# Performance work log

Hardware: AMD Instinct MI355X
Metric: run time of the kernel (lower is better)

## Reference

```python
import jax, jax.numpy as jnp
import numpy as np

B, S, D, H = 4, 4096, 2048, 16
DH = D // H
SCALE = float(np.sqrt(DH))


def setup_inputs() -> dict:
    key = jax.random.key(0)
    ks = jax.random.split(key, 11)
    std = 1.0 / np.sqrt(D)
    inp = {
        "query": jax.random.normal(ks[0], (B, S, D), jnp.float32),
        "key": jax.random.normal(ks[1], (B, S, D), jnp.float32),
        "value": jax.random.normal(ks[2], (B, S, D), jnp.float32),
        "Wq": jax.random.normal(ks[3], (D, D), jnp.float32) * std,
        "bq": jax.random.normal(ks[4], (D,), jnp.float32) * std,
        "Wk": jax.random.normal(ks[5], (D, D), jnp.float32) * std,
        "bk": jax.random.normal(ks[6], (D,), jnp.float32) * std,
        "Wv": jax.random.normal(ks[7], (D, D), jnp.float32) * std,
        "bv": jax.random.normal(ks[8], (D,), jnp.float32) * std,
        "Wo": jax.random.normal(ks[9], (D, D), jnp.float32) * std,
        "bo": jax.random.normal(ks[10], (D,), jnp.float32) * std,
    }
    return inp


def reference(query, key, value, Wq, bq, Wk, bk, Wv, bv, Wo, bo):
    # Linear projections (torch nn.Linear: x @ W^T + b)
    Q = query @ Wq.T + bq          # [B,S,D]
    K = key @ Wk.T + bk
    V = value @ Wv.T + bv
    Q = Q.reshape(B, S, H, DH)
    K = K.reshape(B, S, H, DH)
    V = V.reshape(B, S, H, DH)
    # NOTE: original torch code does NOT transpose heads to dim 1, so the
    # matmul contracts over head-dim pairs at each position: scores [B,S,H,H]
    scores = jnp.einsum('bsid,bsjd->bsij', Q, K) / SCALE
    attention = jax.nn.softmax(scores, axis=-1)   # softmax over heads (faithful)
    x = jnp.einsum('bsij,bsjd->bsid', attention, V)  # [B,S,H,DH]
    # permute(0,2,1,3) -> [B,H,S,DH], then view(B,-1,D) -> [B,S,D]
    x = jnp.transpose(x, (0, 2, 1, 3)).reshape(B, S, D)
    out = x @ Wo.T + bo
    return out, attention
```

## Files before the change

kernel.cpp:

```cpp
#include <hip/hip_runtime.h>


#define DEV __device__ __forceinline__

using short8  = __attribute__((ext_vector_type(8))) short;
using ushort8 = __attribute__((ext_vector_type(8))) unsigned short;
using f32x4   = __attribute__((ext_vector_type(4))) float;
using u16x8   = __attribute__((ext_vector_type(8))) unsigned short;

constexpr int BATCH = 4, SEQ = 4096, DIM = 2048;
constexpr int GM = BATCH * SEQ;
constexpr int GN = DIM, GK = DIM;

DEV unsigned short f2bf(float f) {
  unsigned int u = __builtin_bit_cast(unsigned int, f);
  u += 0x7FFFu + ((u >> 16) & 1u);
  return (unsigned short)(u >> 16);
}
DEV float bf2f(unsigned short h) {
  unsigned int u = ((unsigned int)h) << 16;
  return __builtin_bit_cast(float, u);
}

DEV void gload16(const void* g, void* l) {
  __builtin_amdgcn_global_load_lds(
      (const __attribute__((address_space(1))) void*)g,
      (__attribute__((address_space(3))) void*)l, 16, 0, 0);
}

#define BAR    __builtin_amdgcn_s_barrier()
#define LGKM0  asm volatile("s_waitcnt lgkmcnt(0)" ::: "memory")
#define LGKM(N) asm volatile("s_waitcnt lgkmcnt(" #N ")" ::: "memory")
#define VMC(N) asm volatile("s_waitcnt vmcnt(" #N ")" ::: "memory")
#define SCHED0 __builtin_amdgcn_sched_barrier(0)
#define PRIO1  __builtin_amdgcn_s_setprio(1)
#define PRIO0  __builtin_amdgcn_s_setprio(0)
#define MFMA16(a, b, c) __builtin_amdgcn_mfma_f32_16x16x32_bf16(a, b, c, 0, 0, 0)

#define QUAD(AF, BF, MO, NO)                                          \
  _Pragma("unroll") for (int m_ = 0; m_ < 4; ++m_)                    \
  _Pragma("unroll") for (int n_ = 0; n_ < 4; ++n_) {                  \
    acc[(MO) + m_][(NO) + n_] =                                       \
        MFMA16(AF[m_][0], BF[n_][0], acc[(MO) + m_][(NO) + n_]);      \
    acc[(MO) + m_][(NO) + n_] =                                       \
        MFMA16(AF[m_][1], BF[n_][1], acc[(MO) + m_][(NO) + n_]);      \
  }

constexpr size_t NE_C = (size_t)GM * GK;
constexpr size_t WE_C = (size_t)GK * GN;

__global__ __launch_bounds__(256)
void cvt_all(const float* __restrict__ q, const float* __restrict__ k,
             const float* __restrict__ v, const float* __restrict__ Wq,
             const float* __restrict__ Wk, const float* __restrict__ Wv,
             const float* __restrict__ Wo,
             unsigned short* __restrict__ Qin, unsigned short* __restrict__ Kin,
             unsigned short* __restrict__ Vin, unsigned short* __restrict__ Wqb,
             unsigned short* __restrict__ Wkb, unsigned short* __restrict__ Wvb,
             unsigned short* __restrict__ Wob) {
  size_t gi = ((size_t)blockIdx.x * 256 + threadIdx.x) * 8;
  const float* src;
  unsigned short* dst;
  size_t off;
  if (gi < NE_C)            { src = q;  dst = Qin; off = gi; }
  else if (gi < 2 * NE_C)   { src = k;  dst = Kin; off = gi - NE_C; }
  else if (gi < 3 * NE_C)   { src = v;  dst = Vin; off = gi - 2 * NE_C; }
  else {
    size_t w = gi - 3 * NE_C;
    if (w < WE_C)           { src = Wq; dst = Wqb; off = w; }
    else if (w < 2 * WE_C)  { src = Wk; dst = Wkb; off = w - WE_C; }
    else if (w < 3 * WE_C)  { src = Wv; dst = Wvb; off = w - 2 * WE_C; }
    else                    { src = Wo; dst = Wob; off = w - 3 * WE_C; }
  }
  f32x4 f0 = *(const f32x4*)(src + off);
  f32x4 f1 = *(const f32x4*)(src + off + 4);
  ushort8 o;
#pragma unroll
  for (int j = 0; j < 4; ++j) { o[j] = f2bf(f0[j]); o[4 + j] = f2bf(f1[j]); }
  *(ushort8*)(dst + off) = o;
}

template <bool OUTF32>
__global__ __launch_bounds__(256, 1)
void gemm256p(const unsigned short* __restrict__ Ap,
              const unsigned short* __restrict__ Bp,
              const float* __restrict__ bias, void* __restrict__ Cp) {
  constexpr int BK = 64, KT = GK / BK;
  __shared__ unsigned short As[2][256 * BK];
  __shared__ unsigned short Bs[2][256 * BK];

  const int tid  = threadIdx.x;
  const int lane = tid & 63;
  const int wv   = tid >> 6;
  const int wm   = wv >> 1, wn = wv & 1;

  int bid = (int)blockIdx.x;
  const int xcd = bid & 7, rr = bid >> 3;
  const int gg = rr >> 5, jj = rr & 31;
  const int mt = xcd * 8 + gg * 4 + (jj & 3);
  const int nt = jj >> 2;
  const int bm0 = mt * 256, bn0 = nt * 256;

  int offA[8];
#pragma unroll
  for (int r = 0; r < 8; ++r) {
    int d = tid * 16 + r * 4096;
    int s = d ^ (((d >> 7) & 7) << 4);
    int row = s >> 7, col = (s & 127) >> 1;
    offA[r] = (bm0 + row) * GK + col;
  }
  const int dAB = (bn0 - bm0) * GK;

  const int r16 = lane & 15, kb = (lane >> 4) * 16;

  f32x4 acc[8][8] = {};
  short8 al[4][2], ah[4][2], bl[4][2], bh[4][2];

  auto stA = [&](int buf, int T) {
#pragma unroll
    for (int r = 0; r < 8; ++r)
      gload16(Ap + (size_t)offA[r] + (size_t)T * BK,
              (char*)&As[buf][0] + (tid * 16 + r * 4096));
  };
  auto stB = [&](int buf, int T) {
#pragma unroll
    for (int r = 0; r < 8; ++r)
      gload16(Bp + (size_t)(offA[r] + dAB) + (size_t)T * BK,
              (char*)&Bs[buf][0] + (tid * 16 + r * 4096));
  };
  auto ldf = [&](const unsigned short* base, int row, int ks) -> short8 {
    int a = (row * 128 + ks * 64 + kb) ^ ((row & 7) << 4);
    return *(const short8*)((const char*)base + a);
  };
  auto rdS = [&](short8 (&dst)[4][2], const unsigned short* base, int row0) {
#pragma unroll
    for (int m = 0; m < 4; ++m) {
      dst[m][0] = ldf(base, row0 + m * 16 + r16, 0);
      dst[m][1] = ldf(base, row0 + m * 16 + r16, 1);
    }
  };

  stA(0, 0); stB(0, 0);
  VMC(0); SCHED0; BAR;
  stA(1, 1); stB(1, 1);
  rdS(al, &As[0][0], wm * 128);
  rdS(bl, &Bs[0][0], wn * 128);

  for (int T = 0; T < KT; ++T) {
    const int bb = T & 1;
    const unsigned short* Ac = &As[bb][0];
    const unsigned short* Bc = &Bs[bb][0];
    const unsigned short* An = &As[bb ^ 1][0];
    const unsigned short* Bn = &Bs[bb ^ 1][0];
    const bool m1 = (T + 1 < KT), m2 = (T + 2 < KT);

    rdS(bh, Bc, wn * 128 + 64);
    LGKM(8); SCHED0;
    PRIO1; QUAD(al, bl, 0, 0); PRIO0;

    rdS(ah, Ac, wm * 128 + 64);
    LGKM(8); SCHED0;
    PRIO1; QUAD(al, bh, 0, 4); PRIO0;

    LGKM0; SCHED0;
    if (m1) {
      if (m2) { VMC(8); } else { VMC(0); }
      SCHED0; BAR;
      if (m2) stA(bb, T + 2);
      rdS(al, An, wm * 128);
    }
    PRIO1; QUAD(ah, bh, 4, 4); PRIO0;

    if (m1) {
      if (m2) { VMC(8); } else { VMC(0); }
      SCHED0; BAR;
      if (m2) stB(bb, T + 2);
    }
    PRIO1; QUAD(ah, bl, 4, 0); PRIO0;
    if (m1) rdS(bl, Bn, wn * 128);
  }

  float bs[8];
#pragma unroll
  for (int n = 0; n < 8; ++n) bs[n] = bias[bn0 + wn * 128 + n * 16 + r16];
  const int rb = (lane >> 4) * 4;
#pragma unroll
  for (int m = 0; m < 8; ++m)
#pragma unroll
    for (int i = 0; i < 4; ++i) {
      const size_t row = (size_t)bm0 + wm * 128 + m * 16 + rb + i;
#pragma unroll
      for (int n = 0; n < 8; ++n) {
        const int col = bn0 + wn * 128 + n * 16 + r16;
        float v = acc[m][n][i] + bs[n];
        if constexpr (OUTF32)
          ((float*)Cp)[row * GN + col] = v;
        else
          ((unsigned short*)Cp)[row * GN + col] = f2bf(v);
      }
    }
}

__global__ __launch_bounds__(256)
void attn_kernel(const unsigned short* __restrict__ Qb,
                 const unsigned short* __restrict__ Kb,
                 const unsigned short* __restrict__ Vb,
                 float* __restrict__ attnOut,
                 unsigned short* __restrict__ X2) {
  __shared__ float qf[16 * 128];
  __shared__ float kf[16 * 132];
  __shared__ float vf[16 * 128];
  __shared__ float sc[256];

  const int t = threadIdx.x;
  const int p = blockIdx.x;
  const size_t rowoff = (size_t)p * DIM;

  {
    const int e = t * 8;
    u16x8 qv = *(const u16x8*)(Qb + rowoff + e);
    u16x8 kv = *(const u16x8*)(Kb + rowoff + e);
    u16x8 vv = *(const u16x8*)(Vb + rowoff + e);
    const int r = t >> 4, c = (t & 15) * 8;
#pragma unroll
    for (int j = 0; j < 8; ++j) qf[r * 128 + c + j] = bf2f(qv[j]);
#pragma unroll
    for (int j = 0; j < 8; ++j) kf[r * 132 + c + j] = bf2f(kv[j]);
#pragma unroll
    for (int j = 0; j < 8; ++j) vf[r * 128 + c + j] = bf2f(vv[j]);
  }
  __syncthreads();

  const int i = t >> 4, j = t & 15;
  float s = 0.f;
#pragma unroll
  for (int d4 = 0; d4 < 32; ++d4) {
    f32x4 q4 = *(const f32x4*)&qf[i * 128 + d4 * 4];
    f32x4 k4 = *(const f32x4*)&kf[j * 132 + d4 * 4];
    s = fmaf(q4[0], k4[0], fmaf(q4[1], k4[1], fmaf(q4[2], k4[2], fmaf(q4[3], k4[3], s))));
  }
  s *= 0.08838834764831845f;

  float mx = s;
#pragma unroll
  for (int off = 8; off; off >>= 1) mx = fmaxf(mx, __shfl_xor(mx, off, 16));
  float ex = __expf(s - mx);
  float sum = ex;
#pragma unroll
  for (int off = 8; off; off >>= 1) sum += __shfl_xor(sum, off, 16);
  float a = ex / sum;

  attnOut[(size_t)p * 256 + t] = a;
  sc[t] = a;
  __syncthreads();

  const int dh0 = j * 8;
  float o[8] = {};
#pragma unroll
  for (int jjq = 0; jjq < 16; ++jjq) {
    float aij = sc[i * 16 + jjq];
#pragma unroll
    for (int e2 = 0; e2 < 8; ++e2)
      o[e2] = fmaf(aij, vf[jjq * 128 + dh0 + e2], o[e2]);
  }
  const int b = p >> 12, spos = p & 4095;
  const int row = i * 256 + (spos >> 4);
  const int col = ((spos & 15) << 7) + dh0;
  ushort8 pk;
#pragma unroll
  for (int e2 = 0; e2 < 8; ++e2) pk[e2] = f2bf(o[e2]);
  *(ushort8*)(X2 + (size_t)b * (SEQ * DIM) + (size_t)row * DIM + col) = pk;
}

extern "C" void kernel_launch(void* const* d_in, const int* in_sizes, int n_in,
                              void* d_out, int out_size, void* d_ws,
                              size_t ws_size, hipStream_t stream) {
  const float* q  = (const float*)d_in[0];
  const float* k  = (const float*)d_in[1];
  const float* v  = (const float*)d_in[2];
  const float* Wq = (const float*)d_in[3];
  const float* bq = (const float*)d_in[4];
  const float* Wk = (const float*)d_in[5];
  const float* bk = (const float*)d_in[6];
  const float* Wv = (const float*)d_in[7];
  const float* bv = (const float*)d_in[8];
  const float* Wo = (const float*)d_in[9];
  const float* bo = (const float*)d_in[10];

  const size_t NE = NE_C;
  const size_t WE = WE_C;

  unsigned short* ws16 = (unsigned short*)d_ws;
  unsigned short* Wq_b = ws16;
  unsigned short* Wk_b = Wq_b + WE;
  unsigned short* Wv_b = Wk_b + WE;
  unsigned short* Wo_b = Wv_b + WE;
  unsigned short* Qb   = Wo_b + WE;
  unsigned short* Kb   = Qb + NE;
  unsigned short* Vb   = Kb + NE;
  unsigned short* X2   = Vb + NE;
  unsigned short* Qin  = X2 + NE;
  unsigned short* Kin  = Qin + NE;
  unsigned short* Vin  = Kin + NE;

  float* outMain = (float*)d_out;
  float* attnOut = outMain + (size_t)GM * GN;

  const int cvt_blocks = (int)((3 * NE + 4 * WE) / 8 / 256);
  cvt_all<<<cvt_blocks, 256, 0, stream>>>(q, k, v, Wq, Wk, Wv, Wo,
                                          Qin, Kin, Vin, Wq_b, Wk_b, Wv_b, Wo_b);

  constexpr int G256 = (GM / 256) * (GN / 256);

  gemm256p<false><<<G256, 256, 0, stream>>>(Qin, Wq_b, bq, Qb);
  gemm256p<false><<<G256, 256, 0, stream>>>(Kin, Wk_b, bk, Kb);
  gemm256p<false><<<G256, 256, 0, stream>>>(Vin, Wv_b, bv, Vb);

  attn_kernel<<<GM, 256, 0, stream>>>(Qb, Kb, Vb, attnOut, X2);

  gemm256p<true><<<G256, 256, 0, stream>>>(X2, Wo_b, bo, outMain);
}
```

Before: 950.7 us.

## Pre-swizzle weights into MFMA fragment layout and load B directly to registers

The weight conversion kernel now writes the weights in an MFMA-fragment-ordered layout, so each wave can load its B operand straight from global memory into registers. The LDS staging path for B is dropped. The GEMM tile shrinks from 256x256 to 128x128, uses a triple-buffered LDS ring for A only, and targets two blocks per CU. This cuts LDS traffic and barriers and raises occupancy, at the cost of more global B reads per tile and a smaller per-block reuse footprint.

```diff
diff --git a/kernel.cpp b/kernel.cpp
--- a/kernel.cpp
+++ b/kernel.cpp
@@ -29,174 +29,177 @@
 }
 
 #define BAR    __builtin_amdgcn_s_barrier()
-#define LGKM0  asm volatile("s_waitcnt lgkmcnt(0)" ::: "memory")
-#define LGKM(N) asm volatile("s_waitcnt lgkmcnt(" #N ")" ::: "memory")
 #define VMC(N) asm volatile("s_waitcnt vmcnt(" #N ")" ::: "memory")
 #define SCHED0 __builtin_amdgcn_sched_barrier(0)
 #define PRIO1  __builtin_amdgcn_s_setprio(1)
 #define PRIO0  __builtin_amdgcn_s_setprio(0)
 #define MFMA16(a, b, c) __builtin_amdgcn_mfma_f32_16x16x32_bf16(a, b, c, 0, 0, 0)
 
-#define QUAD(AF, BF, MO, NO)                                          \
-  _Pragma("unroll") for (int m_ = 0; m_ < 4; ++m_)                    \
-  _Pragma("unroll") for (int n_ = 0; n_ < 4; ++n_) {                  \
-    acc[(MO) + m_][(NO) + n_] =                                       \
-        MFMA16(AF[m_][0], BF[n_][0], acc[(MO) + m_][(NO) + n_]);      \
-    acc[(MO) + m_][(NO) + n_] =                                       \
-        MFMA16(AF[m_][1], BF[n_][1], acc[(MO) + m_][(NO) + n_]);      \
-  }
-
 constexpr size_t NE_C = (size_t)GM * GK;
 constexpr size_t WE_C = (size_t)GK * GN;
 
 __global__ __launch_bounds__(256)
-void cvt_all(const float* __restrict__ q, const float* __restrict__ k,
-             const float* __restrict__ v, const float* __restrict__ Wq,
-             const float* __restrict__ Wk, const float* __restrict__ Wv,
-             const float* __restrict__ Wo,
-             unsigned short* __restrict__ Qin, unsigned short* __restrict__ Kin,
-             unsigned short* __restrict__ Vin, unsigned short* __restrict__ Wqb,
-             unsigned short* __restrict__ Wkb, unsigned short* __restrict__ Wvb,
-             unsigned short* __restrict__ Wob) {
-  size_t gi = ((size_t)blockIdx.x * 256 + threadIdx.x) * 8;
-  const float* src;
-  unsigned short* dst;
-  size_t off;
-  if (gi < NE_C)            { src = q;  dst = Qin; off = gi; }
-  else if (gi < 2 * NE_C)   { src = k;  dst = Kin; off = gi - NE_C; }
-  else if (gi < 3 * NE_C)   { src = v;  dst = Vin; off = gi - 2 * NE_C; }
-  else {
-    size_t w = gi - 3 * NE_C;
-    if (w < WE_C)           { src = Wq; dst = Wqb; off = w; }
-    else if (w < 2 * WE_C)  { src = Wk; dst = Wkb; off = w - WE_C; }
-    else if (w < 3 * WE_C)  { src = Wv; dst = Wvb; off = w - 2 * WE_C; }
-    else                    { src = Wo; dst = Wob; off = w - 3 * WE_C; }
-  }
-  f32x4 f0 = *(const f32x4*)(src + off);
-  f32x4 f1 = *(const f32x4*)(src + off + 4);
-  ushort8 o;
-#pragma unroll
-  for (int j = 0; j < 4; ++j) { o[j] = f2bf(f0[j]); o[4 + j] = f2bf(f1[j]); }
-  *(ushort8*)(dst + off) = o;
+void prep(const float* __restrict__ q, const float* __restrict__ k,
+          const float* __restrict__ v, const float* __restrict__ Wq,
+          const float* __restrict__ Wk, const float* __restrict__ Wv,
+          const float* __restrict__ Wo,
+          unsigned short* __restrict__ Qin, unsigned short* __restrict__ Kin,
+          unsigned short* __restrict__ Vin, unsigned short* __restrict__ Bq,
+          unsigned short* __restrict__ Bk, unsigned short* __restrict__ Bv,
+          unsigned short* __restrict__ Bo) {
+  const int bid = blockIdx.x;
+  if (bid < 49152) {
+    const int tens = bid >> 14;
+    const size_t off = ((size_t)(bid & 16383) * 256 + threadIdx.x) * 8;
+    const float* s = tens == 0 ? q : tens == 1 ? k : v;
+    unsigned short* d = tens == 0 ? Qin : tens == 1 ? Kin : Vin;
+    f32x4 f0 = *(const f32x4*)(s + off);
+    f32x4 f1 = *(const f32x4*)(s + off + 4);
+    ushort8 o;
+#pragma unroll
+    for (int j = 0; j < 4; ++j) { o[j] = f2bf(f0[j]); o[4 + j] = f2bf(f1[j]); }
+    *(ushort8*)(d + off) = o;
+  } else {
+    const int wb = bid - 49152;
+    const int w = wb >> 11;
+    const int t = (wb & 2047) * 256 + threadIdx.x;
+    const float* W = w == 0 ? Wq : w == 1 ? Wk : w == 2 ? Wv : Wo;
+    unsigned short* D = w == 0 ? Bq : w == 1 ? Bk : w == 2 ? Bv : Bo;
+    const int lane = t & 63, f = (t >> 6) & 7, half = (t >> 9) & 1;
+    const int kt = (t >> 10) & 31, nt = t >> 15;
+    const int n  = nt * 128 + half * 64 + (f >> 1) * 16 + (lane & 15);
+    const int kk = kt * 64 + (f & 1) * 32 + (lane >> 4) * 8;
+    const float* sp = W + (size_t)n * GK + kk;
+    f32x4 f0 = *(const f32x4*)sp;
+    f32x4 f1 = *(const f32x4*)(sp + 4);
+    ushort8 o;
+#pragma unroll
+    for (int j = 0; j < 4; ++j) { o[j] = f2bf(f0[j]); o[4 + j] = f2bf(f1[j]); }
+    *(ushort8*)(D + (size_t)t * 8) = o;
+  }
 }
 
 template <bool OUTF32>
-__global__ __launch_bounds__(256, 1)
-void gemm256p(const unsigned short* __restrict__ Ap,
-              const unsigned short* __restrict__ Bp,
+__global__ __launch_bounds__(256, 2)
+void gemm128d(const unsigned short* __restrict__ Ap,
+              const unsigned short* __restrict__ Bf,
               const float* __restrict__ bias, void* __restrict__ Cp) {
   constexpr int BK = 64, KT = GK / BK;
-  __shared__ unsigned short As[2][256 * BK];
-  __shared__ unsigned short Bs[2][256 * BK];
+  __shared__ unsigned short As[3][128 * 64];
 
   const int tid  = threadIdx.x;
   const int lane = tid & 63;
   const int wv   = tid >> 6;
   const int wm   = wv >> 1, wn = wv & 1;
 
-  int bid = (int)blockIdx.x;
+  const int bid = (int)blockIdx.x;
   const int xcd = bid & 7, rr = bid >> 3;
-  const int gg = rr >> 5, jj = rr & 31;
-  const int mt = xcd * 8 + gg * 4 + (jj & 3);
-  const int nt = jj >> 2;
-  const int bm0 = mt * 256, bn0 = nt * 256;
-
-  int offA[8];
-#pragma unroll
-  for (int r = 0; r < 8; ++r) {
+  const int gg = rr >> 6, jj = rr & 63;
+  const int mt = xcd * 16 + (gg >> 1) * 8 + (jj & 7);
+  const int nt = (gg & 1) * 8 + (jj >> 3);
+  const int bm0 = mt * 128, bn0 = nt * 128;
+
+  int offA[4];
+#pragma unroll
+  for (int r = 0; r < 4; ++r) {
     int d = tid * 16 + r * 4096;
     int s = d ^ (((d >> 7) & 7) << 4);
-    int row = s >> 7, col = (s & 127) >> 1;
-    offA[r] = (bm0 + row) * GK + col;
-  }
-  const int dAB = (bn0 - bm0) * GK;
-
+    offA[r] = (bm0 + (s >> 7)) * GK + ((s & 127) >> 1);
+  }
   const int r16 = lane & 15, kb = (lane >> 4) * 16;
 
-  f32x4 acc[8][8] = {};
-  short8 al[4][2], ah[4][2], bl[4][2], bh[4][2];
-
-  auto stA = [&](int buf, int T) {
-#pragma unroll
-    for (int r = 0; r < 8; ++r)
+  const unsigned short* Bw =
+      Bf + (size_t)nt * KT * 8192 + (size_t)wn * 4096 + (size_t)lane * 8;
+
+  f32x4 acc[4][4] = {};
+  short8 afA[4][2], afB[4][2], bA[4][2], bB[4][2];
+
+  auto stA = [&](int bufoff, int T) {
+#pragma unroll
+    for (int r = 0; r < 4; ++r)
       gload16(Ap + (size_t)offA[r] + (size_t)T * BK,
-              (char*)&As[buf][0] + (tid * 16 + r * 4096));
-  };
-  auto stB = [&](int buf, int T) {
-#pragma unroll
-    for (int r = 0; r < 8; ++r)
-      gload16(Bp + (size_t)(offA[r] + dAB) + (size_t)T * BK,
-              (char*)&Bs[buf][0] + (tid * 16 + r * 4096));
-  };
-  auto ldf = [&](const unsigned short* base, int row, int ks) -> short8 {
-    int a = (row * 128 + ks * 64 + kb) ^ ((row & 7) << 4);
-    return *(const short8*)((const char*)base + a);
-  };
-  auto rdS = [&](short8 (&dst)[4][2], const unsigned short* base, int row0) {
-#pragma unroll
-    for (int m = 0; m < 4; ++m) {
-      dst[m][0] = ldf(base, row0 + m * 16 + r16, 0);
-      dst[m][1] = ldf(base, row0 + m * 16 + r16, 1);
+              (char*)&As[0][0] + bufoff + (tid * 16 + r * 4096));
+  };
+  auto loadB = [&](short8 (&b)[4][2], int T) {
+    const unsigned short* p = Bw + (size_t)T * 8192;
+#pragma unroll
+    for (int f = 0; f < 8; ++f) {
+      asm volatile("global_load_dwordx4 %0, %1, off"
+                   : "=v"(b[f >> 1][f & 1]) : "v"(p + f * 512) : "memory");
     }
   };
-
-  stA(0, 0); stB(0, 0);
-  VMC(0); SCHED0; BAR;
-  stA(1, 1); stB(1, 1);
-  rdS(al, &As[0][0], wm * 128);
-  rdS(bl, &Bs[0][0], wn * 128);
-
-  for (int T = 0; T < KT; ++T) {
-    const int bb = T & 1;
-    const unsigned short* Ac = &As[bb][0];
-    const unsigned short* Bc = &Bs[bb][0];
-    const unsigned short* An = &As[bb ^ 1][0];
-    const unsigned short* Bn = &Bs[bb ^ 1][0];
-    const bool m1 = (T + 1 < KT), m2 = (T + 2 < KT);
-
-    rdS(bh, Bc, wn * 128 + 64);
-    LGKM(8); SCHED0;
-    PRIO1; QUAD(al, bl, 0, 0); PRIO0;
-
-    rdS(ah, Ac, wm * 128 + 64);
-    LGKM(8); SCHED0;
-    PRIO1; QUAD(al, bh, 0, 4); PRIO0;
-
-    LGKM0; SCHED0;
-    if (m1) {
-      if (m2) { VMC(8); } else { VMC(0); }
-      SCHED0; BAR;
-      if (m2) stA(bb, T + 2);
-      rdS(al, An, wm * 128);
+  auto rdA = [&](short8 (&a)[4][2], int bufoff) {
+#pragma unroll
+    for (int m = 0; m < 4; ++m)
+#pragma unroll
+      for (int ks = 0; ks < 2; ++ks) {
+        int row = wm * 64 + m * 16 + r16;
+        int ad = (row * 128 + ks * 64 + kb) ^ ((row & 7) << 4);
+        a[m][ks] = *(const short8*)((const char*)&As[0][0] + bufoff + ad);
+      }
+  };
+  auto cluster = [&](short8 (&a)[4][2], short8 (&b)[4][2]) {
+    PRIO1;
+#pragma unroll
+    for (int m = 0; m < 4; ++m)
+#pragma unroll
+      for (int n = 0; n < 4; ++n) {
+        acc[m][n] = MFMA16(a[m][0], b[n][0], acc[m][n]);
+        acc[m][n] = MFMA16(a[m][1], b[n][1], acc[m][n]);
+      }
+    PRIO0;
+  };
+
+  auto body = [&](int T, short8 (&cb)[4][2], short8 (&nb)[4][2],
+                  short8 (&ca)[4][2], short8 (&na)[4][2],
+                  int bufn, int bufs) {
+    if (T + 1 < KT) loadB(nb, T + 1);
+    SCHED0;
+    if (T + 2 < KT) stA(bufs, T + 2);
+    SCHED0;
+    if (T + 2 < KT)      { VMC(12); }
+    else if (T + 1 < KT) { VMC(8); }
+    else                 { VMC(0); }
+    SCHED0;
+    if (T + 1 < KT) {
+      BAR; SCHED0;
+      rdA(na, bufn);
+      SCHED0;
     }
-    PRIO1; QUAD(ah, bh, 4, 4); PRIO0;
-
-    if (m1) {
-      if (m2) { VMC(8); } else { VMC(0); }
-      SCHED0; BAR;
-      if (m2) stB(bb, T + 2);
-    }
-    PRIO1; QUAD(ah, bl, 4, 0); PRIO0;
-    if (m1) rdS(bl, Bn, wn * 128);
-  }
-
-  float bs[8];
-#pragma unroll
-  for (int n = 0; n < 8; ++n) bs[n] = bias[bn0 + wn * 128 + n * 16 + r16];
+    cluster(ca, cb);
+  };
+
+  stA(0, 0); stA(16384, 1);
+  loadB(bA, 0);
+  SCHED0; VMC(12); SCHED0;
+  BAR; SCHED0;
+  rdA(afA, 0);
+  SCHED0;
+
+  int b0 = 0, b1 = 16384, b2 = 32768;
+  for (int T = 0; T < KT; T += 2) {
+    body(T,     bA, bB, afA, afB, b1, b2);
+    body(T + 1, bB, bA, afB, afA, b2, b0);
+    int tmp = b2; b2 = b1; b1 = b0; b0 = tmp;
+  }
+
+  float bs[4];
+#pragma unroll
+  for (int n = 0; n < 4; ++n) bs[n] = bias[bn0 + wn * 64 + n * 16 + r16];
   const int rb = (lane >> 4) * 4;
 #pragma unroll
-  for (int m = 0; m < 8; ++m)
+  for (int m = 0; m < 4; ++m)
 #pragma unroll
     for (int i = 0; i < 4; ++i) {
-      const size_t row = (size_t)bm0 + wm * 128 + m * 16 + rb + i;
-#pragma unroll
-      for (int n = 0; n < 8; ++n) {
-        const int col = bn0 + wn * 128 + n * 16 + r16;
-        float v = acc[m][n][i] + bs[n];
+      const size_t row = (size_t)bm0 + wm * 64 + m * 16 + rb + i;
+#pragma unroll
+      for (int n = 0; n < 4; ++n) {
+        const int col = bn0 + wn * 64 + n * 16 + r16;
+        float val = acc[m][n][i] + bs[n];
         if constexpr (OUTF32)
-          ((float*)Cp)[row * GN + col] = v;
+          ((float*)Cp)[row * GN + col] = val;
         else
-          ((unsigned short*)Cp)[row * GN + col] = f2bf(v);
+          ((unsigned short*)Cp)[row * GN + col] = f2bf(val);
       }
     }
 }
@@ -287,15 +290,14 @@
   const float* Wo = (const float*)d_in[9];
   const float* bo = (const float*)d_in[10];
 
-  const size_t NE = NE_C;
-  const size_t WE = WE_C;
+  const size_t NE = NE_C, WE = WE_C;
 
   unsigned short* ws16 = (unsigned short*)d_ws;
-  unsigned short* Wq_b = ws16;
-  unsigned short* Wk_b = Wq_b + WE;
-  unsigned short* Wv_b = Wk_b + WE;
-  unsigned short* Wo_b = Wv_b + WE;
-  unsigned short* Qb   = Wo_b + WE;
+  unsigned short* Bq_f = ws16;
+  unsigned short* Bk_f = Bq_f + WE;
+  unsigned short* Bv_f = Bk_f + WE;
+  unsigned short* Bo_f = Bv_f + WE;
+  unsigned short* Qb   = Bo_f + WE;
   unsigned short* Kb   = Qb + NE;
   unsigned short* Vb   = Kb + NE;
   unsigned short* X2   = Vb + NE;
@@ -306,17 +308,16 @@
   float* outMain = (float*)d_out;
   float* attnOut = outMain + (size_t)GM * GN;
 
-  const int cvt_blocks = (int)((3 * NE + 4 * WE) / 8 / 256);
-  cvt_all<<<cvt_blocks, 256, 0, stream>>>(q, k, v, Wq, Wk, Wv, Wo,
-                                          Qin, Kin, Vin, Wq_b, Wk_b, Wv_b, Wo_b);
-
-  constexpr int G256 = (GM / 256) * (GN / 256);
-
-  gemm256p<false><<<G256, 256, 0, stream>>>(Qin, Wq_b, bq, Qb);
-  gemm256p<false><<<G256, 256, 0, stream>>>(Kin, Wk_b, bk, Kb);
-  gemm256p<false><<<G256, 256, 0, stream>>>(Vin, Wv_b, bv, Vb);
+  prep<<<57344, 256, 0, stream>>>(q, k, v, Wq, Wk, Wv, Wo,
+                                  Qin, Kin, Vin, Bq_f, Bk_f, Bv_f, Bo_f);
+
+  constexpr int G128 = (GM / 128) * (GN / 128);
+
+  gemm128d<false><<<G128, 256, 0, stream>>>(Qin, Bq_f, bq, Qb);
+  gemm128d<false><<<G128, 256, 0, stream>>>(Kin, Bk_f, bk, Kb);
+  gemm128d<false><<<G128, 256, 0, stream>>>(Vin, Bv_f, bv, Vb);
 
   attn_kernel<<<GM, 256, 0, stream>>>(Qb, Kb, Vb, attnOut, X2);
 
-  gemm256p<true><<<G256, 256, 0, stream>>>(X2, Wo_b, bo, outMain);
-}
+  gemm128d<true><<<G128, 256, 0, stream>>>(X2, Bo_f, bo, outMain);
+}
```

Result: faster. 817.0 us (-14.1%).

## Rework projection GEMM into 8-wave four-stage pipeline and fuse QKV launches

Applied to the files above, without the earlier changes.

Replaces the 4-wave, double-buffered 256x256 GEMM (BK=64) with an 8-wave version that uses BK=32 and a four-buffer pipeline. Loads are prefetched three k-steps ahead and each wave computes a 128x64 sub-tile. The three Q/K/V projections now run as one launch that picks its tensor from the block index, which removes launch gaps and tail effects between them. The trade-off is more barriers per k-step and 128KB of LDS, so the requested two blocks per CU likely cannot both fit.

```diff
diff --git a/kernel.cpp b/kernel.cpp
--- a/kernel.cpp
+++ b/kernel.cpp
@@ -30,21 +30,11 @@
 
 #define BAR    __builtin_amdgcn_s_barrier()
 #define LGKM0  asm volatile("s_waitcnt lgkmcnt(0)" ::: "memory")
-#define LGKM(N) asm volatile("s_waitcnt lgkmcnt(" #N ")" ::: "memory")
 #define VMC(N) asm volatile("s_waitcnt vmcnt(" #N ")" ::: "memory")
 #define SCHED0 __builtin_amdgcn_sched_barrier(0)
 #define PRIO1  __builtin_amdgcn_s_setprio(1)
 #define PRIO0  __builtin_amdgcn_s_setprio(0)
 #define MFMA16(a, b, c) __builtin_amdgcn_mfma_f32_16x16x32_bf16(a, b, c, 0, 0, 0)
-
-#define QUAD(AF, BF, MO, NO)                                          \
-  _Pragma("unroll") for (int m_ = 0; m_ < 4; ++m_)                    \
-  _Pragma("unroll") for (int n_ = 0; n_ < 4; ++n_) {                  \
-    acc[(MO) + m_][(NO) + n_] =                                       \
-        MFMA16(AF[m_][0], BF[n_][0], acc[(MO) + m_][(NO) + n_]);      \
-    acc[(MO) + m_][(NO) + n_] =                                       \
-        MFMA16(AF[m_][1], BF[n_][1], acc[(MO) + m_][(NO) + n_]);      \
-  }
 
 constexpr size_t NE_C = (size_t)GM * GK;
 constexpr size_t WE_C = (size_t)GK * GN;
@@ -80,109 +70,119 @@
   *(ushort8*)(dst + off) = o;
 }
 
-template <bool OUTF32>
-__global__ __launch_bounds__(256, 1)
-void gemm256p(const unsigned short* __restrict__ Ap,
-              const unsigned short* __restrict__ Bp,
-              const float* __restrict__ bias, void* __restrict__ Cp) {
-  constexpr int BK = 64, KT = GK / BK;
-  __shared__ unsigned short As[2][256 * BK];
-  __shared__ unsigned short Bs[2][256 * BK];
+template <bool OUTF32, bool MULTI>
+__global__ __launch_bounds__(512, 2)
+void gemm_d(const unsigned short* __restrict__ A0,
+            const unsigned short* __restrict__ A1,
+            const unsigned short* __restrict__ A2,
+            const unsigned short* __restrict__ B0,
+            const unsigned short* __restrict__ B1,
+            const unsigned short* __restrict__ B2,
+            const float* __restrict__ bi0, const float* __restrict__ bi1,
+            const float* __restrict__ bi2,
+            void* __restrict__ C0, void* __restrict__ C1,
+            void* __restrict__ C2) {
+  constexpr int BK = 32, KT = GK / BK;
+  __shared__ unsigned short As[4][256 * BK];
+  __shared__ unsigned short Bs[4][256 * BK];
 
   const int tid  = threadIdx.x;
   const int lane = tid & 63;
   const int wv   = tid >> 6;
-  const int wm   = wv >> 1, wn = wv & 1;
-
-  int bid = (int)blockIdx.x;
+  const int wm   = wv >> 2, wn = wv & 3;
+
+  const int bid = (int)blockIdx.x;
   const int xcd = bid & 7, rr = bid >> 3;
-  const int gg = rr >> 5, jj = rr & 31;
+  const int tens = MULTI ? (rr >> 6) : 0;
+  const int r2 = MULTI ? (rr & 63) : rr;
+  const int gg = r2 >> 5, jj = r2 & 31;
   const int mt = xcd * 8 + gg * 4 + (jj & 3);
   const int nt = jj >> 2;
   const int bm0 = mt * 256, bn0 = nt * 256;
 
-  int offA[8];
-#pragma unroll
-  for (int r = 0; r < 8; ++r) {
-    int d = tid * 16 + r * 4096;
-    int s = d ^ (((d >> 7) & 7) << 4);
-    int row = s >> 7, col = (s & 127) >> 1;
-    offA[r] = (bm0 + row) * GK + col;
-  }
-  const int dAB = (bn0 - bm0) * GK;
-
-  const int r16 = lane & 15, kb = (lane >> 4) * 16;
-
-  f32x4 acc[8][8] = {};
-  short8 al[4][2], ah[4][2], bl[4][2], bh[4][2];
-
-  auto stA = [&](int buf, int T) {
-#pragma unroll
-    for (int r = 0; r < 8; ++r)
-      gload16(Ap + (size_t)offA[r] + (size_t)T * BK,
-              (char*)&As[buf][0] + (tid * 16 + r * 4096));
+  const unsigned short* Ap = tens == 0 ? A0 : tens == 1 ? A1 : A2;
+  const unsigned short* Bp = tens == 0 ? B0 : tens == 1 ? B1 : B2;
+  const float* bias        = tens == 0 ? bi0 : tens == 1 ? bi1 : bi2;
+  void* Cp                 = tens == 0 ? C0 : tens == 1 ? C1 : C2;
+
+  int offA[2], offB[2];
+#pragma unroll
+  for (int r = 0; r < 2; ++r) {
+    int d = tid * 16 + r * 8192;
+    int line = d >> 7;
+    int qq = (d & 127) ^ ((line & 7) << 4);
+    int row = line * 2 + (qq >> 6);
+    int c = qq & 63;
+    offA[r] = (bm0 + row) * GK + (c >> 1);
+    offB[r] = (bn0 + row) * GK + (c >> 1);
+  }
+
+  const int r16 = lane & 15;
+  const int kb = (lane >> 4) * 16;
+
+  f32x4 acc[8][4] = {};
+  short8 af[4], bf[4];
+
+  auto stage = [&](const unsigned short* P, void* lbase, int T, int* offs) {
+#pragma unroll
+    for (int r = 0; r < 2; ++r)
+      gload16(P + (size_t)offs[r] + (size_t)T * BK,
+              (char*)lbase + (tid * 16 + r * 8192));
   };
-  auto stB = [&](int buf, int T) {
-#pragma unroll
-    for (int r = 0; r < 8; ++r)
-      gload16(Bp + (size_t)(offA[r] + dAB) + (size_t)T * BK,
-              (char*)&Bs[buf][0] + (tid * 16 + r * 4096));
+  auto frag = [&](const unsigned short* lbase, int row) -> short8 {
+    int line = row >> 1;
+    int ad = line * 128 + ((((row & 1) << 6) + kb) ^ ((line & 7) << 4));
+    return *(const short8*)((const char*)lbase + ad);
   };
-  auto ldf = [&](const unsigned short* base, int row, int ks) -> short8 {
-    int a = (row * 128 + ks * 64 + kb) ^ ((row & 7) << 4);
-    return *(const short8*)((const char*)base + a);
-  };
-  auto rdS = [&](short8 (&dst)[4][2], const unsigned short* base, int row0) {
-#pragma unroll
-    for (int m = 0; m < 4; ++m) {
-      dst[m][0] = ldf(base, row0 + m * 16 + r16, 0);
-      dst[m][1] = ldf(base, row0 + m * 16 + r16, 1);
-    }
-  };
-
-  stA(0, 0); stB(0, 0);
-  VMC(0); SCHED0; BAR;
-  stA(1, 1); stB(1, 1);
-  rdS(al, &As[0][0], wm * 128);
-  rdS(bl, &Bs[0][0], wn * 128);
+
+  stage(Ap, &As[0][0], 0, offA); stage(Bp, &Bs[0][0], 0, offB);
+  stage(Ap, &As[1][0], 1, offA); stage(Bp, &Bs[1][0], 1, offB);
+  stage(Ap, &As[2][0], 2, offA); stage(Bp, &Bs[2][0], 2, offB);
+  VMC(8);
+  BAR;
 
   for (int T = 0; T < KT; ++T) {
-    const int bb = T & 1;
-    const unsigned short* Ac = &As[bb][0];
-    const unsigned short* Bc = &Bs[bb][0];
-    const unsigned short* An = &As[bb ^ 1][0];
-    const unsigned short* Bn = &Bs[bb ^ 1][0];
-    const bool m1 = (T + 1 < KT), m2 = (T + 2 < KT);
-
-    rdS(bh, Bc, wn * 128 + 64);
-    LGKM(8); SCHED0;
-    PRIO1; QUAD(al, bl, 0, 0); PRIO0;
-
-    rdS(ah, Ac, wm * 128 + 64);
-    LGKM(8); SCHED0;
-    PRIO1; QUAD(al, bh, 0, 4); PRIO0;
-
-    LGKM0; SCHED0;
-    if (m1) {
-      if (m2) { VMC(8); } else { VMC(0); }
-      SCHED0; BAR;
-      if (m2) stA(bb, T + 2);
-      rdS(al, An, wm * 128);
-    }
-    PRIO1; QUAD(ah, bh, 4, 4); PRIO0;
-
-    if (m1) {
-      if (m2) { VMC(8); } else { VMC(0); }
-      SCHED0; BAR;
-      if (m2) stB(bb, T + 2);
-    }
-    PRIO1; QUAD(ah, bl, 4, 0); PRIO0;
-    if (m1) rdS(bl, Bn, wn * 128);
-  }
-
-  float bs[8];
-#pragma unroll
-  for (int n = 0; n < 8; ++n) bs[n] = bias[bn0 + wn * 128 + n * 16 + r16];
+    const int buf = T & 3, nxt = (T + 3) & 3;
+    const unsigned short* Ab = &As[buf][0];
+    const unsigned short* Bb = &Bs[buf][0];
+    const bool pf = (T + 3 < KT);
+
+#pragma unroll
+    for (int m = 0; m < 4; ++m) af[m] = frag(Ab, wm * 128 + m * 16 + r16);
+#pragma unroll
+    for (int n = 0; n < 4; ++n) bf[n] = frag(Bb, wn * 64 + n * 16 + r16);
+    SCHED0;
+    if (pf) stage(Ap, &As[nxt][0], T + 3, offA);
+    SCHED0; BAR; LGKM0; SCHED0;
+    PRIO1;
+#pragma unroll
+    for (int m = 0; m < 4; ++m)
+#pragma unroll
+      for (int n = 0; n < 4; ++n)
+        acc[m][n] = MFMA16(af[m], bf[n], acc[m][n]);
+    PRIO0; SCHED0; BAR;
+
+#pragma unroll
+    for (int m = 0; m < 4; ++m) af[m] = frag(Ab, wm * 128 + 64 + m * 16 + r16);
+    SCHED0;
+    if (pf) stage(Bp, &Bs[nxt][0], T + 3, offB);
+    SCHED0;
+    if (pf)                 { VMC(8); }
+    else if (T + 2 < KT)    { VMC(4); }
+    else                    { VMC(0); }
+    SCHED0; BAR; LGKM0; SCHED0;
+    PRIO1;
+#pragma unroll
+    for (int m = 0; m < 4; ++m)
+#pragma unroll
+      for (int n = 0; n < 4; ++n)
+        acc[4 + m][n] = MFMA16(af[m], bf[n], acc[4 + m][n]);
+    PRIO0; SCHED0; BAR;
+  }
+
+  float bs[4];
+#pragma unroll
+  for (int n = 0; n < 4; ++n) bs[n] = bias[bn0 + wn * 64 + n * 16 + r16];
   const int rb = (lane >> 4) * 4;
 #pragma unroll
   for (int m = 0; m < 8; ++m)
@@ -190,8 +190,8 @@
     for (int i = 0; i < 4; ++i) {
       const size_t row = (size_t)bm0 + wm * 128 + m * 16 + rb + i;
 #pragma unroll
-      for (int n = 0; n < 8; ++n) {
-        const int col = bn0 + wn * 128 + n * 16 + r16;
+      for (int n = 0; n < 4; ++n) {
+        const int col = bn0 + wn * 64 + n * 16 + r16;
         float v = acc[m][n][i] + bs[n];
         if constexpr (OUTF32)
           ((float*)Cp)[row * GN + col] = v;
@@ -287,8 +287,7 @@
   const float* Wo = (const float*)d_in[9];
   const float* bo = (const float*)d_in[10];
 
-  const size_t NE = NE_C;
-  const size_t WE = WE_C;
+  const size_t NE = NE_C, WE = WE_C;
 
   unsigned short* ws16 = (unsigned short*)d_ws;
   unsigned short* Wq_b = ws16;
@@ -310,13 +309,12 @@
   cvt_all<<<cvt_blocks, 256, 0, stream>>>(q, k, v, Wq, Wk, Wv, Wo,
                                           Qin, Kin, Vin, Wq_b, Wk_b, Wv_b, Wo_b);
 
-  constexpr int G256 = (GM / 256) * (GN / 256);
-
-  gemm256p<false><<<G256, 256, 0, stream>>>(Qin, Wq_b, bq, Qb);
-  gemm256p<false><<<G256, 256, 0, stream>>>(Kin, Wk_b, bk, Kb);
-  gemm256p<false><<<G256, 256, 0, stream>>>(Vin, Wv_b, bv, Vb);
+  gemm_d<false, true><<<1536, 512, 0, stream>>>(
+      Qin, Kin, Vin, Wq_b, Wk_b, Wv_b, bq, bk, bv, Qb, Kb, Vb);
 
   attn_kernel<<<GM, 256, 0, stream>>>(Qb, Kb, Vb, attnOut, X2);
 
-  gemm256p<true><<<G256, 256, 0, stream>>>(X2, Wo_b, bo, outMain);
-}
+  gemm_d<true, false><<<512, 512, 0, stream>>>(
+      X2, nullptr, nullptr, Wo_b, nullptr, nullptr, bo, nullptr, nullptr,
+      outMain, nullptr, nullptr);
+}
```

Result: faster. 818.5 us (median of 2 runs) (-13.9%).
